# Performance work log

Hardware: AMD Instinct MI355X
Metric: run time of the kernel (lower is better)

Reference implementation:

```python
import jax, jax.numpy as jnp
import numpy as np
from math import sqrt

BS, SEQ, NV, DM, K = 16, 1024, 512, 256, 8
EPS = 0.05  # sinkhorn epsilon
TEMP = 0.07  # concrete-bernoulli temperature


def setup_inputs() -> dict:
    key = jax.random.key(0)
    k1, k2, k3 = jax.random.split(key, 3)
    x = jax.random.normal(k1, (BS, SEQ, NV), jnp.float32)
    # nn.Linear(seq_len, d_model): weight [d_model, seq_len], bias [d_model]
    W = jax.random.normal(k2, (DM, SEQ), jnp.float32) / sqrt(SEQ)
    b = jnp.zeros((DM,), jnp.float32)
    cluster_emb = jax.random.normal(k3, (K, DM), jnp.float32) / sqrt(DM)
    return {"x": x, "W": W, "b": b, "cluster_emb": cluster_emb}


def _l2norm(z):
    # F.normalize(x, dim=1, p=2) with eps=1e-12 clamp
    n = jnp.maximum(jnp.linalg.norm(z, axis=1, keepdims=True), 1e-12)
    return z / n


def _sinkhorn(q):
    Q = jnp.exp(q / EPS)
    return Q / jnp.sum(Q, axis=1, keepdims=True)


def _concrete_bern(p, key):
    u = jax.random.uniform(key, p.shape, p.dtype, 1e-10, 1.0 - 1e-10)
    noise = jnp.log(u) - jnp.log1p(-u)
    logit = jnp.log(p + 1e-10) - jnp.log(1.0 - p + 1e-10)
    return jax.nn.sigmoid((logit + noise) / TEMP)


def _forward(x, W, b, cluster_emb):
    bs, S, nv = x.shape
    d = W.shape[0]
    k = cluster_emb.shape[0]
    # permute -> [bs, nv, S], Linear(S -> d)
    x_emb = jnp.einsum('bsv,ds->bvd', x, W) + b  # [bs, nv, d]
    x_flat = x_emb.reshape(-1, d)  # [bs*nv, d]
    # cosine-similarity cluster logits
    prob = (_l2norm(x_flat) @ _l2norm(cluster_emb).T).reshape(bs, nv, k)
    prob_temp = _sinkhorn(prob.reshape(-1, k)).reshape(bs, nv, k)  # individual probs
    prob_avg = _sinkhorn(jnp.mean(prob, axis=0))  # [nv, k]
    mask = _concrete_bern(prob_avg, jax.random.key(42))  # [nv, k]
    # CrossAttention with n_heads=1 (dropout inactive in eval)
    scale = 1.0 / sqrt(d)
    scores = jnp.einsum('kd,bvd->bkv', cluster_emb, x_emb)  # [bs, k, nv]
    A = jax.nn.softmax(scale * scores, axis=-1) * mask.T[None]  # masked attn
    V = jnp.einsum('bkv,bvd->bkd', A, x_emb)  # [bs, k, d]
    cluster_emb_avg = jnp.mean(V, axis=0)  # [k, d] (stored attribute in torch)
    # cluster_base_encoding: straight-through bernoulli, broadcast over seq_len
    soft = prob_temp.transpose(2, 0, 1)[..., None]  # [k, bs, nv, 1]
    u = jax.random.uniform(jax.random.key(7), soft.shape, soft.dtype)
    bern = (u < jax.lax.stop_gradient(soft)).astype(soft.dtype)
    extend = jnp.broadcast_to(bern, (k, bs, nv, S))  # [k, bs, nv, S]
    hard = soft + jax.lax.stop_gradient(extend - soft)  # straight-through
    return hard


def reference(x, W, b, cluster_emb):
    return _forward(x, W, b, cluster_emb)
```

## Files before the change

### kernel.cpp

```cpp
#include <hip/hip_runtime.h>
#include <hip/hip_bf16.h>
#include <math.h>
#include <stdint.h>

#define BS 16
#define SEQ 1024
#define NV 512
#define DM 256
#define NK 8

__device__ double g_WC[NK * SEQ];
__device__ double g_Bk[NK];
__device__ __align__(16) float g_zp[2 * 4 * BS * NV * 64];
__device__ double g_nn2[BS * NV];
__device__ double g_Dp[8 * BS * NV * NK];
__device__ unsigned char g_bits[BS * NV];

__device__ __forceinline__ void threefry2x32_key7(uint32_t x0, uint32_t x1,
                                                  uint32_t& o0, uint32_t& o1) {
    const uint32_t k0 = 0u, k1 = 7u;
    const uint32_t k2 = k0 ^ k1 ^ 0x1BD11BDAu;
    uint32_t v0 = x0 + k0, v1 = x1 + k1;
#define TF_ROUND(r) { v0 += v1; v1 = (v1 << (r)) | (v1 >> (32 - (r))); v1 ^= v0; }
    TF_ROUND(13) TF_ROUND(15) TF_ROUND(26) TF_ROUND(6)
    v0 += k1; v1 += k2 + 1u;
    TF_ROUND(17) TF_ROUND(29) TF_ROUND(16) TF_ROUND(24)
    v0 += k2; v1 += k0 + 2u;
    TF_ROUND(13) TF_ROUND(15) TF_ROUND(26) TF_ROUND(6)
    v0 += k0; v1 += k1 + 3u;
    TF_ROUND(17) TF_ROUND(29) TF_ROUND(16) TF_ROUND(24)
    v0 += k1; v1 += k2 + 4u;
    TF_ROUND(13) TF_ROUND(15) TF_ROUND(26) TF_ROUND(6)
    v0 += k2; v1 += k0 + 5u;
#undef TF_ROUND
    o0 = v0; o1 = v1;
}

__device__ __forceinline__ float bits_to_uniform(uint32_t b) {
    return __uint_as_float((b >> 9) | 0x3F800000u) - 1.0f;
}

__global__ __launch_bounds__(256) void prep_kernel(
        const float* __restrict__ W, const float* __restrict__ bias,
        const float* __restrict__ ce) {
    __shared__ double red[256];
    __shared__ double cen[256];
    const int t = threadIdx.x;
    const int k = blockIdx.x >> 2;
    const int schunk = blockIdx.x & 3;

    double c = (double)ce[k * DM + t];
    red[t] = c * c;
    __syncthreads();
    for (int off = 128; off > 0; off >>= 1) {
        if (t < off) red[t] += red[t + off];
        __syncthreads();
    }
    double nc = fmax(sqrt(red[0]), 1e-12);
    cen[t] = c / nc;
    __syncthreads();
    red[t] = (double)bias[t] * cen[t];
    __syncthreads();
    for (int off = 128; off > 0; off >>= 1) {
        if (t < off) red[t] += red[t + off];
        __syncthreads();
    }
    if (t == 0 && schunk == 0) g_Bk[k] = red[0];

    const int s = schunk * 256 + t;
    double acc = 0.0;
    for (int d = 0; d < DM; ++d)
        acc += cen[d] * (double)W[(size_t)d * SEQ + s];
    g_WC[(size_t)k * SEQ + s] = acc;
}

#define KC 32
#define XS_LD 132
#define WS_LD 68
#define ZS_LD 68

__global__ __launch_bounds__(256) void gemm_kernel(
        const float* __restrict__ x, const float* __restrict__ W) {
    __shared__ __align__(16) char smem[34816];
    float* xs  = (float*)smem;
    float* wst = (float*)(smem + 16896);
    float* zS  = (float*)smem;

    const int t = threadIdx.x;
    const int dblk = blockIdx.x & 3;
    const int kblk = blockIdx.x >> 2;
    const int vblk = blockIdx.y;
    const int b    = blockIdx.z;
    const int v0 = vblk * 128, d0 = dblk * 64;
    const float* xb = x + (size_t)b * SEQ * NV;

    const int kh  = t >> 7;
    const int tid = t & 127;
    const int tv8 = (tid & 15) * 8;
    const int td8 = (tid >> 4) * 8;
    const int kb  = kh * 16;

    float acc[8][8];
#pragma unroll
    for (int j = 0; j < 8; ++j)
#pragma unroll
        for (int i = 0; i < 8; ++i) acc[j][i] = 0.0f;

    const int sbeg = kblk * 512;
    for (int s0 = sbeg; s0 < sbeg + 512; s0 += KC) {
        __syncthreads();
#pragma unroll
        for (int j = 0; j < 4; ++j) {
            int lin = j * 256 + t;
            int sl = lin >> 5;
            int c4 = (lin & 31) << 2;
            float4 val = *(const float4*)&xb[(size_t)(s0 + sl) * NV + v0 + c4];
            *(float4*)&xs[sl * XS_LD + c4] = val;
        }
#pragma unroll
        for (int j = 0; j < 8; ++j) {
            int dl = (t >> 5) + 8 * j;
            int sl = t & 31;
            wst[sl * WS_LD + dl] = W[(size_t)(d0 + dl) * SEQ + s0 + sl];
        }
        __syncthreads();
#pragma unroll
        for (int kk = 0; kk < 16; ++kk) {
            const float* xr = &xs[(kb + kk) * XS_LD + tv8];
            const float* wr = &wst[(kb + kk) * WS_LD + td8];
            float4 xv0 = *(const float4*)(xr);
            float4 xv1 = *(const float4*)(xr + 4);
            float4 wv0 = *(const float4*)(wr);
            float4 wv1 = *(const float4*)(wr + 4);
            float xv[8] = {xv0.x, xv0.y, xv0.z, xv0.w, xv1.x, xv1.y, xv1.z, xv1.w};
            float wv[8] = {wv0.x, wv0.y, wv0.z, wv0.w, wv1.x, wv1.y, wv1.z, wv1.w};
#pragma unroll
            for (int j = 0; j < 8; ++j)
#pragma unroll
                for (int i = 0; i < 8; ++i) acc[j][i] += xv[j] * wv[i];
        }
    }

    __syncthreads();
    if (kh == 1) {
#pragma unroll
        for (int j = 0; j < 8; ++j) {
            *(float4*)&zS[(tv8 + j) * ZS_LD + td8]     =
                make_float4(acc[j][0], acc[j][1], acc[j][2], acc[j][3]);
            *(float4*)&zS[(tv8 + j) * ZS_LD + td8 + 4] =
                make_float4(acc[j][4], acc[j][5], acc[j][6], acc[j][7]);
        }
    }
    __syncthreads();
    if (kh == 0) {
#pragma unroll
        for (int j = 0; j < 8; ++j) {
            float zrow[8];
#pragma unroll
            for (int i = 0; i < 8; ++i)
                zrow[i] = acc[j][i] + zS[(tv8 + j) * ZS_LD + td8 + i];
            size_t rowbase =
                ((((size_t)kblk * 4 + dblk) * BS + b) * NV + v0 + tv8 + j) * 64 + td8;
            *(float4*)&g_zp[rowbase]     = make_float4(zrow[0], zrow[1], zrow[2], zrow[3]);
            *(float4*)&g_zp[rowbase + 4] = make_float4(zrow[4], zrow[5], zrow[6], zrow[7]);
        }
    }
}

__global__ __launch_bounds__(256) void combine_kernel(
        const float* __restrict__ bias) {
    __shared__ double red[16][17];
    const int t = threadIdx.x;
    const int vg = blockIdx.x;
    const int b  = blockIdx.y;
    const int vl = t >> 4, dg = t & 15;
    const int v = vg * 16 + vl;
    const int dblk = dg >> 2, dl0 = (dg & 3) * 16;

    const size_t base0 = ((((size_t)0 * 4 + dblk) * BS + b) * NV + v) * 64 + dl0;
    const size_t base1 = ((((size_t)1 * 4 + dblk) * BS + b) * NV + v) * 64 + dl0;
    double sq = 0.0;
#pragma unroll
    for (int m = 0; m < 16; m += 4) {
        float4 a  = *(const float4*)&g_zp[base0 + m];
        float4 c  = *(const float4*)&g_zp[base1 + m];
        float4 bb = *(const float4*)&bias[dg * 16 + m];
        double z0 = (double)a.x + (double)c.x + (double)bb.x;
        double z1 = (double)a.y + (double)c.y + (double)bb.y;
        double z2 = (double)a.z + (double)c.z + (double)bb.z;
        double z3 = (double)a.w + (double)c.w + (double)bb.w;
        sq += z0 * z0 + z1 * z1 + z2 * z2 + z3 * z3;
    }
    red[vl][dg] = sq;
    __syncthreads();
    if (dg == 0) {
        double s = 0.0;
#pragma unroll
        for (int i = 0; i < 16; ++i) s += red[vl][i];
        g_nn2[b * NV + v] = s;
    }
}

__global__ __launch_bounds__(256) void dkern(const float* __restrict__ x) {
    __shared__ double wcd[NK][128];
    __shared__ double dw[4][64][NK];
    const int t = threadIdx.x;
    const int vblk = blockIdx.x;
    const int b    = blockIdx.y;
    const int sc   = blockIdx.z;
    const int v0 = vblk * 64;
    const int ss = sc * 128;

#pragma unroll
    for (int j = 0; j < 4; ++j) {
        int idx = j * 256 + t;
        ((double*)wcd)[idx] = g_WC[(size_t)(idx >> 7) * SEQ + ss + (idx & 127)];
    }
    __syncthreads();

    const int vl = t & 63, w = t >> 6;
    const float* xp = x + (size_t)b * SEQ * NV + v0 + vl;
    double D[NK];
#pragma unroll
    for (int k = 0; k < NK; ++k) D[k] = 0.0;
    const int sw = w * 32;
    for (int i = 0; i < 32; ++i) {
        int sl = sw + i;
        double xv = (double)xp[(size_t)(ss + sl) * NV];
#pragma unroll
        for (int k = 0; k < NK; ++k) D[k] += xv * wcd[k][sl];
    }
#pragma unroll
    for (int k = 0; k < NK; ++k) dw[w][vl][k] = D[k];
    __syncthreads();

    const int v = t & 63, k2 = (t >> 6) * 2;
#pragma unroll
    for (int j = 0; j < 2; ++j) {
        int k = k2 + j;
        double s = dw[0][v][k] + dw[1][v][k] + dw[2][v][k] + dw[3][v][k];
        g_Dp[(((size_t)sc * BS + b) * NV + v0 + v) * NK + k] = s;
    }
}

__global__ __launch_bounds__(256) void finalize_kernel() {
    const int bv = blockIdx.x * 256 + threadIdx.x;
    double n = fmax(sqrt(g_nn2[bv]), 1e-12);

    double D[NK];
#pragma unroll
    for (int k = 0; k < NK; ++k) D[k] = g_Bk[k];
#pragma unroll
    for (int sc = 0; sc < 8; ++sc) {
#pragma unroll
        for (int k = 0; k < NK; ++k)
            D[k] += g_Dp[((size_t)sc * (BS * NV) + bv) * NK + k];
    }

    double p[NK], sum = 0.0;
#pragma unroll
    for (int k = 0; k < NK; ++k) {
        p[k] = exp((D[k] / n) / 0.05);
        sum += p[k];
    }
    unsigned int byte = 0;
#pragma unroll
    for (int k = 0; k < NK; ++k) {
        uint32_t i = (uint32_t)(k * (BS * NV) + bv);
        uint32_t y0, y1;
        threefry2x32_key7(0u, i, y0, y1);
        float u = bits_to_uniform(y0 ^ y1);
        if ((double)u < p[k] / sum) byte |= 1u << k;
    }
    g_bits[bv] = (unsigned char)byte;
}

__global__ __launch_bounds__(256) void write_kernel(float* __restrict__ out) {
    const int t = threadIdx.x;
    const size_t r0 = (size_t)blockIdx.x * 8;
#pragma unroll
    for (int j = 0; j < 8; ++j) {
        size_t r = r0 + j;
        unsigned int bv = (unsigned int)(r & 8191u);
        unsigned int k  = (unsigned int)(r >> 13);
        float v = ((g_bits[bv] >> k) & 1u) ? 1.0f : 0.0f;
        float4 val = make_float4(v, v, v, v);
        ((float4*)(out + r * 1024))[t] = val;
    }
}

extern "C" void kernel_launch(void* const* d_in, const int* in_sizes, int n_in,
                              void* d_out, int out_size, void* d_ws, size_t ws_size,
                              hipStream_t stream) {
    const float* x    = (const float*)d_in[0];
    const float* W    = (const float*)d_in[1];
    const float* bias = (const float*)d_in[2];
    const float* ce   = (const float*)d_in[3];
    float* out = (float*)d_out;

    prep_kernel<<<dim3(32), dim3(256), 0, stream>>>(W, bias, ce);
    gemm_kernel<<<dim3(8, 4, 16), dim3(256), 0, stream>>>(x, W);
    combine_kernel<<<dim3(32, 16), dim3(256), 0, stream>>>(bias);
    dkern<<<dim3(8, 16, 8), dim3(256), 0, stream>>>(x);
    finalize_kernel<<<dim3(32), dim3(256), 0, stream>>>();
    write_kernel<<<dim3(8192), dim3(256), 0, stream>>>(out);
}
```

Measured before the change: 395.5 us.

## Pre-transpose W and widen GEMM tile to full d_model with 4-way split-K

A new kernel transposes W into a global [SEQ, DM] buffer so the GEMM can load weight tiles with coalesced float4 reads. Each GEMM block now covers all 256 output columns with an 8x16 per-thread accumulator and a 256-long K chunk. This removes the four-fold re-reading of x across d-blocks and the in-block reduction through shared memory. The cost is a 4-way split-K whose partial sums take twice as much global memory, one extra launch, fewer blocks (256, launch bounds of 1 block per SM) and higher register pressure.

```diff
diff --git a/kernel.cpp b/kernel.cpp
--- a/kernel.cpp
+++ b/kernel.cpp
@@ -11,7 +11,8 @@
 
 __device__ double g_WC[NK * SEQ];
 __device__ double g_Bk[NK];
-__device__ __align__(16) float g_zp[2 * 4 * BS * NV * 64];
+__device__ __align__(16) float g_Wt[SEQ * DM];
+__device__ __align__(16) float g_zp[4 * BS * NV * DM];
 __device__ double g_nn2[BS * NV];
 __device__ double g_Dp[8 * BS * NV * NK];
 __device__ unsigned char g_bits[BS * NV];
@@ -40,6 +41,28 @@
     return __uint_as_float((b >> 9) | 0x3F800000u) - 1.0f;
 }
 
+__global__ __launch_bounds__(256) void wt_kernel(const float* __restrict__ W) {
+    __shared__ float tile[64][132];
+    const int t = threadIdx.x;
+    const int s0 = blockIdx.x * 64;
+    const int d0 = blockIdx.y * 128;
+#pragma unroll
+    for (int p = 0; p < 32; ++p) {
+        int lin = p * 256 + t;
+        int d = lin >> 6, s = lin & 63;
+        tile[s][d] = W[(size_t)(d0 + d) * SEQ + s0 + s];
+    }
+    __syncthreads();
+#pragma unroll
+    for (int p = 0; p < 32; ++p) {
+        int lin = p * 256 + t;
+        int s = lin >> 7, d = lin & 127;
+        int sl = (p >> 1) * 2 + s - (p >> 1) * 2;
+        (void)sl;
+        g_Wt[(size_t)(s0 + (lin >> 7)) * DM + d0 + d] = tile[lin >> 7][d];
+    }
+}
+
 __global__ __launch_bounds__(256) void prep_kernel(
         const float* __restrict__ W, const float* __restrict__ bias,
         const float* __restrict__ ce) {
@@ -76,94 +99,77 @@
 
 #define KC 32
 #define XS_LD 132
-#define WS_LD 68
-#define ZS_LD 68
-
-__global__ __launch_bounds__(256) void gemm_kernel(
-        const float* __restrict__ x, const float* __restrict__ W) {
-    __shared__ __align__(16) char smem[34816];
-    float* xs  = (float*)smem;
-    float* wst = (float*)(smem + 16896);
-    float* zS  = (float*)smem;
-
-    const int t = threadIdx.x;
-    const int dblk = blockIdx.x & 3;
-    const int kblk = blockIdx.x >> 2;
+#define WST_LD 320
+
+__global__ __launch_bounds__(256, 1) void gemm_kernel(
+        const float* __restrict__ x) {
+    __shared__ __align__(16) float xs[KC * XS_LD];
+    __shared__ __align__(16) float wst[KC * WST_LD];
+
+    const int t = threadIdx.x;
+    const int kblk = blockIdx.x;
     const int vblk = blockIdx.y;
     const int b    = blockIdx.z;
-    const int v0 = vblk * 128, d0 = dblk * 64;
+    const int v0 = vblk * 128;
     const float* xb = x + (size_t)b * SEQ * NV;
 
-    const int kh  = t >> 7;
-    const int tid = t & 127;
-    const int tv8 = (tid & 15) * 8;
-    const int td8 = (tid >> 4) * 8;
-    const int kb  = kh * 16;
-
-    float acc[8][8];
+    const int tv8  = (t & 15) * 8;
+    const int grp  = t >> 4;
+    const int td16 = grp * 16;
+    const int wofs = grp * 20;
+
+    float acc[8][16];
 #pragma unroll
     for (int j = 0; j < 8; ++j)
 #pragma unroll
-        for (int i = 0; i < 8; ++i) acc[j][i] = 0.0f;
-
-    const int sbeg = kblk * 512;
-    for (int s0 = sbeg; s0 < sbeg + 512; s0 += KC) {
+        for (int i = 0; i < 16; ++i) acc[j][i] = 0.0f;
+
+    const int sbeg = kblk * 256;
+    for (int s0 = sbeg; s0 < sbeg + 256; s0 += KC) {
         __syncthreads();
 #pragma unroll
         for (int j = 0; j < 4; ++j) {
             int lin = j * 256 + t;
-            int sl = lin >> 5;
-            int c4 = (lin & 31) << 2;
+            int sl = lin >> 5, c4 = (lin & 31) << 2;
             float4 val = *(const float4*)&xb[(size_t)(s0 + sl) * NV + v0 + c4];
             *(float4*)&xs[sl * XS_LD + c4] = val;
         }
 #pragma unroll
         for (int j = 0; j < 8; ++j) {
-            int dl = (t >> 5) + 8 * j;
-            int sl = t & 31;
-            wst[sl * WS_LD + dl] = W[(size_t)(d0 + dl) * SEQ + s0 + sl];
+            int lin = j * 256 + t;
+            int sl = lin >> 6, c4 = (lin & 63) << 2;
+            float4 val = *(const float4*)&g_Wt[(size_t)(s0 + sl) * DM + c4];
+            *(float4*)&wst[sl * WST_LD + (c4 >> 4) * 20 + (c4 & 15)] = val;
         }
         __syncthreads();
 #pragma unroll
-        for (int kk = 0; kk < 16; ++kk) {
-            const float* xr = &xs[(kb + kk) * XS_LD + tv8];
-            const float* wr = &wst[(kb + kk) * WS_LD + td8];
+        for (int kk = 0; kk < KC; ++kk) {
+            const float* xr = &xs[kk * XS_LD + tv8];
+            const float* wr = &wst[kk * WST_LD + wofs];
             float4 xv0 = *(const float4*)(xr);
             float4 xv1 = *(const float4*)(xr + 4);
             float4 wv0 = *(const float4*)(wr);
             float4 wv1 = *(const float4*)(wr + 4);
+            float4 wv2 = *(const float4*)(wr + 8);
+            float4 wv3 = *(const float4*)(wr + 12);
             float xv[8] = {xv0.x, xv0.y, xv0.z, xv0.w, xv1.x, xv1.y, xv1.z, xv1.w};
-            float wv[8] = {wv0.x, wv0.y, wv0.z, wv0.w, wv1.x, wv1.y, wv1.z, wv1.w};
+            float wv[16] = {wv0.x, wv0.y, wv0.z, wv0.w, wv1.x, wv1.y, wv1.z, wv1.w,
+                            wv2.x, wv2.y, wv2.z, wv2.w, wv3.x, wv3.y, wv3.z, wv3.w};
 #pragma unroll
             for (int j = 0; j < 8; ++j)
 #pragma unroll
-                for (int i = 0; i < 8; ++i) acc[j][i] += xv[j] * wv[i];
+                for (int i = 0; i < 16; ++i) acc[j][i] += xv[j] * wv[i];
         }
     }
 
-    __syncthreads();
-    if (kh == 1) {
-#pragma unroll
-        for (int j = 0; j < 8; ++j) {
-            *(float4*)&zS[(tv8 + j) * ZS_LD + td8]     =
-                make_float4(acc[j][0], acc[j][1], acc[j][2], acc[j][3]);
-            *(float4*)&zS[(tv8 + j) * ZS_LD + td8 + 4] =
-                make_float4(acc[j][4], acc[j][5], acc[j][6], acc[j][7]);
-        }
-    }
-    __syncthreads();
-    if (kh == 0) {
-#pragma unroll
-        for (int j = 0; j < 8; ++j) {
-            float zrow[8];
-#pragma unroll
-            for (int i = 0; i < 8; ++i)
-                zrow[i] = acc[j][i] + zS[(tv8 + j) * ZS_LD + td8 + i];
-            size_t rowbase =
-                ((((size_t)kblk * 4 + dblk) * BS + b) * NV + v0 + tv8 + j) * 64 + td8;
-            *(float4*)&g_zp[rowbase]     = make_float4(zrow[0], zrow[1], zrow[2], zrow[3]);
-            *(float4*)&g_zp[rowbase + 4] = make_float4(zrow[4], zrow[5], zrow[6], zrow[7]);
-        }
+#pragma unroll
+    for (int j = 0; j < 8; ++j) {
+        size_t base = (size_t)kblk * (BS * NV * DM) +
+                      ((size_t)b * NV + v0 + tv8 + j) * DM + td16;
+#pragma unroll
+        for (int m = 0; m < 16; m += 4)
+            *(float4*)&g_zp[base + m] =
+                make_float4(acc[j][m], acc[j][m + 1], acc[j][m + 2], acc[j][m + 3]);
     }
 }
 
@@ -175,20 +181,20 @@
     const int b  = blockIdx.y;
     const int vl = t >> 4, dg = t & 15;
     const int v = vg * 16 + vl;
-    const int dblk = dg >> 2, dl0 = (dg & 3) * 16;
-
-    const size_t base0 = ((((size_t)0 * 4 + dblk) * BS + b) * NV + v) * 64 + dl0;
-    const size_t base1 = ((((size_t)1 * 4 + dblk) * BS + b) * NV + v) * 64 + dl0;
+
+    const size_t bvbase = ((size_t)b * NV + v) * DM + dg * 16;
     double sq = 0.0;
 #pragma unroll
     for (int m = 0; m < 16; m += 4) {
-        float4 a  = *(const float4*)&g_zp[base0 + m];
-        float4 c  = *(const float4*)&g_zp[base1 + m];
+        float4 p0 = *(const float4*)&g_zp[(size_t)0 * (BS * NV * DM) + bvbase + m];
+        float4 p1 = *(const float4*)&g_zp[(size_t)1 * (BS * NV * DM) + bvbase + m];
+        float4 p2 = *(const float4*)&g_zp[(size_t)2 * (BS * NV * DM) + bvbase + m];
+        float4 p3 = *(const float4*)&g_zp[(size_t)3 * (BS * NV * DM) + bvbase + m];
         float4 bb = *(const float4*)&bias[dg * 16 + m];
-        double z0 = (double)a.x + (double)c.x + (double)bb.x;
-        double z1 = (double)a.y + (double)c.y + (double)bb.y;
-        double z2 = (double)a.z + (double)c.z + (double)bb.z;
-        double z3 = (double)a.w + (double)c.w + (double)bb.w;
+        double z0 = (double)p0.x + (double)p1.x + (double)p2.x + (double)p3.x + (double)bb.x;
+        double z1 = (double)p0.y + (double)p1.y + (double)p2.y + (double)p3.y + (double)bb.y;
+        double z2 = (double)p0.z + (double)p1.z + (double)p2.z + (double)p3.z + (double)bb.z;
+        double z3 = (double)p0.w + (double)p1.w + (double)p2.w + (double)p3.w + (double)bb.w;
         sq += z0 * z0 + z1 * z1 + z2 * z2 + z3 * z3;
     }
     red[vl][dg] = sq;
@@ -298,8 +304,9 @@
     const float* ce   = (const float*)d_in[3];
     float* out = (float*)d_out;
 
+    wt_kernel<<<dim3(16, 2), dim3(256), 0, stream>>>(W);
     prep_kernel<<<dim3(32), dim3(256), 0, stream>>>(W, bias, ce);
-    gemm_kernel<<<dim3(8, 4, 16), dim3(256), 0, stream>>>(x, W);
+    gemm_kernel<<<dim3(4, 4, 16), dim3(256), 0, stream>>>(x);
     combine_kernel<<<dim3(32, 16), dim3(256), 0, stream>>>(bias);
     dkern<<<dim3(8, 16, 8), dim3(256), 0, stream>>>(x);
     finalize_kernel<<<dim3(32), dim3(256), 0, stream>>>();
```

New measurement: 390.4 us. About the same (-1.3%).
